# Kernel tuning notes

Measured on AMD Instinct MI355X. Metric: run time of the kernel, lower is better.

The kernel has to match this reference:

```python
import jax, jax.numpy as jnp
import numpy as np

B, T, C, O = 32, 2048, 1152, 29  # batch, temporal len, in channels (sum(data_length)), classes


def setup_inputs() -> dict:
    key = jax.random.key(0)
    k1, k2, k3, k4 = jax.random.split(key, 4)
    x = jax.random.normal(k1, (B, T, C), dtype=jnp.float32)
    # per-sample valid length, >=1 to avoid div-by-zero
    length = jax.random.randint(k2, (B,), 1, T + 1, dtype=jnp.int64)
    # Conv1d(C, O, 1) weight [O, C, 1] -> stored as [O, C]; bias [O]
    W = jax.random.normal(k3, (O, C), dtype=jnp.float32) * (1.0 / np.sqrt(C))
    b = jax.random.normal(k4, (O,), dtype=jnp.float32) * 0.01
    return {"x": x, "length": length, "W": W, "b": b}


def reference(x, length, W, b):
    # x: [B, T, C]; scale/shift then 1x1 conv (pointwise linear) then sum over T.
    # Linearity lets us fuse: sum_t (W @ (x/64 - 2) + b) == einsum + T*b.
    y = x / 64.0 - 2.0                      # [B, T, C]
    z = jnp.einsum('btc,oc->bo', y, W)      # temporal-summed projection [B, O]
    z = z + jnp.asarray(x.shape[1], z.dtype) * b
    return z / length.astype(z.dtype)[:, None]
```

## Files before the change

kernel.cpp:

```cpp
#include <hip/hip_runtime.h>
#include <hip/hip_bf16.h>


#define PB 32
#define PT 2048
#define PC 1152
#define PO 29
#define TSPLIT 32
#define C4 (PC / 4)

__global__ __launch_bounds__(256) void sum_t_kernel(const float* __restrict__ x,
                                                    float* __restrict__ s) {
    const int b   = blockIdx.x;
    const int p   = blockIdx.y;
    const int tid = threadIdx.x;

    const float4* x4 = (const float4*)(x + (size_t)b * PT * PC);

    float4 acc0 = make_float4(0.f, 0.f, 0.f, 0.f);
    float4 acc1 = make_float4(0.f, 0.f, 0.f, 0.f);

    const int tBeg = p * (PT / TSPLIT);
    const int tEnd = tBeg + (PT / TSPLIT);

#pragma unroll 4
    for (int t = tBeg; t < tEnd; ++t) {
        const float4* row = x4 + (size_t)t * C4;
        float4 v = row[tid];
        acc0.x += v.x; acc0.y += v.y; acc0.z += v.z; acc0.w += v.w;
        if (tid < C4 - 256) {
            float4 v2 = row[256 + tid];
            acc1.x += v2.x; acc1.y += v2.y; acc1.z += v2.z; acc1.w += v2.w;
        }
    }

    float* sb = s + b * PC;
    atomicAdd(&sb[tid * 4 + 0], acc0.x);
    atomicAdd(&sb[tid * 4 + 1], acc0.y);
    atomicAdd(&sb[tid * 4 + 2], acc0.z);
    atomicAdd(&sb[tid * 4 + 3], acc0.w);
    if (tid < C4 - 256) {
        atomicAdd(&sb[(256 + tid) * 4 + 0], acc1.x);
        atomicAdd(&sb[(256 + tid) * 4 + 1], acc1.y);
        atomicAdd(&sb[(256 + tid) * 4 + 2], acc1.z);
        atomicAdd(&sb[(256 + tid) * 4 + 3], acc1.w);
    }
}

__global__ __launch_bounds__(64) void proj_kernel(const float* __restrict__ s,
                                                  const float* __restrict__ W,
                                                  const float* __restrict__ bias,
                                                  const int* __restrict__ length,
                                                  float* __restrict__ out) {
    const int o    = blockIdx.x;
    const int b    = blockIdx.y;
    const int lane = threadIdx.x;

    const float* Wo = W + o * PC;
    const float* sb = s + b * PC;

    float dot = 0.f, wsum = 0.f;
#pragma unroll
    for (int c = lane; c < PC; c += 64) {
        float w = Wo[c];
        dot  += w * sb[c];
        wsum += w;
    }

#pragma unroll
    for (int off = 32; off > 0; off >>= 1) {
        dot  += __shfl_down(dot,  off);
        wsum += __shfl_down(wsum, off);
    }

    if (lane == 0) {
        float z = dot * (1.0f / 64.0f)
                - 2.0f * (float)PT * wsum
                + (float)PT * bias[o];
        out[b * PO + o] = z / (float)length[b];
    }
}

extern "C" void kernel_launch(void* const* d_in, const int* in_sizes, int n_in,
                              void* d_out, int out_size, void* d_ws, size_t ws_size,
                              hipStream_t stream) {
    const float* x      = (const float*)d_in[0];
    const int*   length = (const int*)d_in[1];
    const float* W      = (const float*)d_in[2];
    const float* bias   = (const float*)d_in[3];
    float*       out    = (float*)d_out;
    float*       s      = (float*)d_ws;

    hipMemsetAsync(s, 0, (size_t)PB * PC * sizeof(float), stream);

    dim3 g1(PB, TSPLIT);
    sum_t_kernel<<<g1, 256, 0, stream>>>(x, s);

    dim3 g2(PO, PB);
    proj_kernel<<<g2, 64, 0, stream>>>(s, W, bias, length, out);
}
```

Measured before the change: 437.6 us.

## Replace atomics and memset with partial-sum buffer reduced in fused projection kernel

The temporal sum kernel now writes per-slab partial sums to a workspace buffer instead of using atomicAdd, which removes the memset launch. TSPLIT doubles to 64, and x is read with nontemporal loads. A new per-batch kernel reduces the partials into shared memory and computes all 29 outputs, replacing the per-(o,b) projection grid. This adds a small extra pass over the partials and requires a larger workspace.

```diff
diff --git a/kernel.cpp b/kernel.cpp
--- a/kernel.cpp
+++ b/kernel.cpp
@@ -6,78 +6,84 @@
 #define PT 2048
 #define PC 1152
 #define PO 29
-#define TSPLIT 32
+#define TSPLIT 64
+#define SLAB (PT / TSPLIT)
 #define C4 (PC / 4)
 
+typedef float f32x4 __attribute__((ext_vector_type(4)));
+
 __global__ __launch_bounds__(256) void sum_t_kernel(const float* __restrict__ x,
-                                                    float* __restrict__ s) {
+                                                    float* __restrict__ part) {
     const int b   = blockIdx.x;
     const int p   = blockIdx.y;
     const int tid = threadIdx.x;
 
-    const float4* x4 = (const float4*)(x + (size_t)b * PT * PC);
+    const f32x4* x4 = (const f32x4*)(x + (size_t)b * PT * PC)
+                    + (size_t)(p * SLAB) * C4;
 
-    float4 acc0 = make_float4(0.f, 0.f, 0.f, 0.f);
-    float4 acc1 = make_float4(0.f, 0.f, 0.f, 0.f);
+    f32x4 a0 = (f32x4)(0.f);
+    f32x4 a1 = (f32x4)(0.f);
 
-    const int tBeg = p * (PT / TSPLIT);
-    const int tEnd = tBeg + (PT / TSPLIT);
-
-#pragma unroll 4
-    for (int t = tBeg; t < tEnd; ++t) {
-        const float4* row = x4 + (size_t)t * C4;
-        float4 v = row[tid];
-        acc0.x += v.x; acc0.y += v.y; acc0.z += v.z; acc0.w += v.w;
+#pragma unroll 8
+    for (int t = 0; t < SLAB; ++t) {
+        const f32x4* row = x4 + (size_t)t * C4;
+        f32x4 v = __builtin_nontemporal_load(&row[tid]);
+        a0 += v;
         if (tid < C4 - 256) {
-            float4 v2 = row[256 + tid];
-            acc1.x += v2.x; acc1.y += v2.y; acc1.z += v2.z; acc1.w += v2.w;
+            f32x4 v2 = __builtin_nontemporal_load(&row[256 + tid]);
+            a1 += v2;
         }
     }
 
-    float* sb = s + b * PC;
-    atomicAdd(&sb[tid * 4 + 0], acc0.x);
-    atomicAdd(&sb[tid * 4 + 1], acc0.y);
-    atomicAdd(&sb[tid * 4 + 2], acc0.z);
-    atomicAdd(&sb[tid * 4 + 3], acc0.w);
-    if (tid < C4 - 256) {
-        atomicAdd(&sb[(256 + tid) * 4 + 0], acc1.x);
-        atomicAdd(&sb[(256 + tid) * 4 + 1], acc1.y);
-        atomicAdd(&sb[(256 + tid) * 4 + 2], acc1.z);
-        atomicAdd(&sb[(256 + tid) * 4 + 3], acc1.w);
-    }
+    f32x4* out4 = (f32x4*)(part + ((size_t)p * PB + b) * PC);
+    out4[tid] = a0;
+    if (tid < C4 - 256) out4[256 + tid] = a1;
 }
 
-__global__ __launch_bounds__(64) void proj_kernel(const float* __restrict__ s,
-                                                  const float* __restrict__ W,
-                                                  const float* __restrict__ bias,
-                                                  const int* __restrict__ length,
-                                                  float* __restrict__ out) {
-    const int o    = blockIdx.x;
-    const int b    = blockIdx.y;
-    const int lane = threadIdx.x;
+__global__ __launch_bounds__(256) void reduce_proj_kernel(const float* __restrict__ part,
+                                                          const float* __restrict__ W,
+                                                          const float* __restrict__ bias,
+                                                          const int* __restrict__ length,
+                                                          float* __restrict__ out) {
+    __shared__ float s[PC];
+    const int b   = blockIdx.x;
+    const int tid = threadIdx.x;
 
-    const float* Wo = W + o * PC;
-    const float* sb = s + b * PC;
+    const f32x4* part4 = (const f32x4*)part;
+    for (int c4 = tid; c4 < C4; c4 += 256) {
+        f32x4 acc = (f32x4)(0.f);
+#pragma unroll 8
+        for (int p = 0; p < TSPLIT; ++p) {
+            acc += part4[((size_t)p * PB + b) * C4 + c4];
+        }
+        ((f32x4*)s)[c4] = acc;
+    }
+    __syncthreads();
 
-    float dot = 0.f, wsum = 0.f;
+    const int wave = tid >> 6;
+    const int lane = tid & 63;
+    const float invlen = 1.0f / (float)length[b];
+
+    for (int o = wave; o < PO; o += 4) {
+        const float* Wo = W + o * PC;
+        float dot = 0.f, wsum = 0.f;
 #pragma unroll
-    for (int c = lane; c < PC; c += 64) {
-        float w = Wo[c];
-        dot  += w * sb[c];
-        wsum += w;
-    }
-
+        for (int c = lane; c < PC; c += 64) {
+            float w = Wo[c];
+            dot  += w * s[c];
+            wsum += w;
+        }
 #pragma unroll
-    for (int off = 32; off > 0; off >>= 1) {
-        dot  += __shfl_down(dot,  off);
-        wsum += __shfl_down(wsum, off);
-    }
-
-    if (lane == 0) {
-        float z = dot * (1.0f / 64.0f)
-                - 2.0f * (float)PT * wsum
-                + (float)PT * bias[o];
-        out[b * PO + o] = z / (float)length[b];
+        for (int off = 32; off > 0; off >>= 1) {
+            dot  += __shfl_down(dot,  off);
+            wsum += __shfl_down(wsum, off);
+        }
+        if (lane == 0) {
+            float z = dot * (1.0f / 64.0f)
+                    - 2.0f * (float)PT * wsum
+                    + (float)PT * bias[o];
+            out[b * PO + o] = z * invlen;
+        }
     }
 }
 
@@ -89,13 +95,10 @@
     const float* W      = (const float*)d_in[2];
     const float* bias   = (const float*)d_in[3];
     float*       out    = (float*)d_out;
-    float*       s      = (float*)d_ws;
-
-    hipMemsetAsync(s, 0, (size_t)PB * PC * sizeof(float), stream);
+    float*       part   = (float*)d_ws;
 
     dim3 g1(PB, TSPLIT);
-    sum_t_kernel<<<g1, 256, 0, stream>>>(x, s);
+    sum_t_kernel<<<g1, 256, 0, stream>>>(x, part);
 
-    dim3 g2(PO, PB);
-    proj_kernel<<<g2, 64, 0, stream>>>(s, W, bias, length, out);
+    reduce_proj_kernel<<<PB, 256, 0, stream>>>(part, W, bias, length, out);
 }
```

Result: no change. 439.9 us (+0.5%).
